# Performance work log

Hardware: AMD Instinct MI355X
Metric: run time of the kernel (lower is better)

The kernel has to match this reference:

```python
import jax, jax.numpy as jnp
import numpy as np

ATTEN_SIZE = 5  # half-window; module-global atten_size in source (0 there is non-functional)
B, S, D_IN, HID, OUT = 8, 2048, 512, 512, 2


def _xavier(key, shape):
    fan_in, fan_out = shape
    std = (2.0 / (fan_in + fan_out)) ** 0.5
    return jax.random.normal(key, shape, dtype=jnp.float32) * std


def setup_inputs() -> dict:
    key = jax.random.key(0)
    ks = jax.random.split(key, 8)
    return {
        "x": jax.random.normal(ks[0], (B, S, D_IN), dtype=jnp.float32),
        "W1": _xavier(ks[1], (D_IN, HID)),
        "b1": jnp.zeros((1, 1, HID), dtype=jnp.float32),
        "Wq": _xavier(ks[2], (HID, HID)),
        "Wk": _xavier(ks[3], (HID, HID)),
        "Wv": _xavier(ks[4], (HID, HID)),
        "W2": _xavier(ks[5], (HID, HID)),
        "b2": jnp.zeros((1, 1, HID), dtype=jnp.float32),
        "Wfc": _xavier(ks[6], (HID, OUT)),
        "bfc": jnp.zeros((OUT,), dtype=jnp.float32),
    }


def reference(x, W1, b1, Wq, Wk, Wv, W2, b2, Wfc, bfc):
    A = ATTEN_SIZE
    Wn = 2 * A + 1
    h = jax.nn.relu(x @ W1 + b1)                      # [B,S,H]
    b, s, hd = h.shape
    padded = jnp.pad(h, ((0, 0), (A, A), (0, 0)))     # [B,S+2A,H]
    # torch pad+roll(k)+stack+slice equals reversed window: x_nei[p, j] = padded[p + 2A - j]
    idx = jnp.arange(s)[:, None] + (2 * A - jnp.arange(Wn))[None, :]  # [S,Wn]
    x_nei = padded[:, idx, :]                         # [B,S,Wn,H]
    q = h @ Wq                                        # [B,S,H]
    k = x_nei @ Wk                                    # [B,S,Wn,H]
    v = x_nei @ Wv                                    # [B,S,Wn,H]
    scale = jnp.asarray(np.sqrt(float(hd)), dtype=h.dtype)
    scores = jnp.einsum('bsh,bswh->bsw', q, k)[:, :, None, :] / scale  # [B,S,1,Wn]
    # Faithful to torch.nn.Softmax(dim=2) on a singleton dim -> all ones
    w = jax.nn.softmax(scores, axis=2)                # [B,S,1,Wn]
    aw = jnp.einsum('bsjw,bswh->bsjh', w, v).reshape(b, s, hd)  # [B,S,H]
    out = jax.nn.relu(aw @ W2 + b2) @ Wfc + bfc       # [B,S,OUT]
    return out, aw
```

## Files before the change

### kernel.cpp

```cpp
#include <hip/hip_runtime.h>
#include <stdint.h>

#define B_   8
#define S_   2048
#define HID_ 512
#define M_   (B_ * S_)
#define AW_  5

typedef __attribute__((ext_vector_type(8))) short bf16x8;
typedef __attribute__((ext_vector_type(4))) float f32x4;
typedef unsigned short u16;

__device__ __forceinline__ u16 f2bf(float f) {
    uint32_t u = __builtin_bit_cast(uint32_t, f);
    u += 0x7FFFu + ((u >> 16) & 1u);
    return (u16)(u >> 16);
}
__device__ __forceinline__ float bf2f(u16 h) {
    uint32_t u = ((uint32_t)h) << 16;
    return __builtin_bit_cast(float, u);
}

__device__ __forceinline__ void gload16(const void* g, void* l) {
    __builtin_amdgcn_global_load_lds(
        (const __attribute__((address_space(1))) void*)(uintptr_t)g,
        (__attribute__((address_space(3))) void*)(uint32_t)(uintptr_t)l,
        16, 0, 0);
}

#define WAITV(n)  asm volatile("s_waitcnt vmcnt(" #n ")" ::: "memory")
#define WAITLG0() asm volatile("s_waitcnt lgkmcnt(0)" ::: "memory")

__global__ __launch_bounds__(256) void prep_w(const float* __restrict__ W1,
                                              const float* __restrict__ Wv,
                                              const float* __restrict__ W2,
                                              u16* __restrict__ W1t,
                                              u16* __restrict__ Wvt,
                                              u16* __restrict__ W2t,
                                              int do_w2) {
    const int wsel = blockIdx.x >> 8;
    if (wsel == 2 && !do_w2) return;
    const float* src = wsel == 0 ? W1 : (wsel == 1 ? Wv : W2);
    u16* dst = wsel == 0 ? W1t : (wsel == 1 ? Wvt : W2t);
    const int t  = blockIdx.x & 255;
    const int n0 = (t & 15) * 32, k0 = (t >> 4) * 32;
    __shared__ float tile[32][33];
    const int tr = threadIdx.x >> 5, tc = threadIdx.x & 31;
#pragma unroll
    for (int p = 0; p < 4; ++p)
        tile[tr + p * 8][tc] = src[(long)(k0 + tr + p * 8) * HID_ + n0 + tc];
    __syncthreads();
#pragma unroll
    for (int p = 0; p < 4; ++p)
        dst[(long)(n0 + tr + p * 8) * HID_ + k0 + tc] = f2bf(tile[tc][tr + p * 8]);
}

__global__ __launch_bounds__(256) void trans_w2(const float* __restrict__ W2,
                                                u16* __restrict__ W2t) {
    __shared__ float tile[32][33];
    const int k0 = blockIdx.y * 32, n0 = blockIdx.x * 32;
    const int tr = threadIdx.x >> 5, tc = threadIdx.x & 31;
#pragma unroll
    for (int p = 0; p < 4; ++p)
        tile[tr + p * 8][tc] = W2[(long)(k0 + tr + p * 8) * HID_ + n0 + tc];
    __syncthreads();
#pragma unroll
    for (int p = 0; p < 4; ++p)
        W2t[(long)(n0 + tr + p * 8) * HID_ + k0 + tc] = f2bf(tile[tc][tr + p * 8]);
}

__global__ __launch_bounds__(256, 2) void gemm1_f32a(const float* __restrict__ A,
                                                     const u16* __restrict__ Bt,
                                                     const float* __restrict__ bias,
                                                     u16* __restrict__ C) {
    __shared__ __attribute__((aligned(16))) u16 As[2][128 * 64];
    __shared__ __attribute__((aligned(16))) u16 Bs[2][128 * 64];

    const int tid = threadIdx.x;
    const int bid = blockIdx.x;
    const int swz = (bid & 7) * 64 + (bid >> 3);
    const int  bn   = (swz & 3) * 128;
    const long brow = (long)(swz >> 2) * 128;

    const int w  = tid >> 6;
    const int l  = tid & 63;
    const int wm = (w >> 1) * 64;
    const int wn = (w & 1) * 64;
    const int lr  = l & 15;
    const int lkb = (l >> 4) * 16;
    const int sw  = (lr & 7) << 4;

    const int r0 = tid >> 2;
    const int c0 = (tid & 3) * 16;
    const int r1 = 64 + r0;
    const float* ga0 = A + (brow + r0) * 512 + c0;
    const float* ga1 = A + (brow + r1) * 512 + c0;
    char* lw = (char*)&As[0][0];
    const int wb00 = r0 * 128 + ((c0 * 2 +  0) ^ ((r0 & 7) << 4));
    const int wb01 = r0 * 128 + ((c0 * 2 + 16) ^ ((r0 & 7) << 4));
    const int wb10 = r1 * 128 + ((c0 * 2 +  0) ^ ((r1 & 7) << 4));
    const int wb11 = r1 * 128 + ((c0 * 2 + 16) ^ ((r1 & 7) << 4));

    int pq[4];
    const u16* srcB[4];
#pragma unroll
    for (int q = 0; q < 4; ++q) {
        const int p   = tid * 16 + q * 4096;
        const int row = p >> 7;
        const int cb  = (p & 127) ^ ((row & 7) << 4);
        pq[q]   = p;
        srcB[q] = Bt + (long)(bn + row) * 512 + (cb >> 1);
    }

    f32x4 acc[4][4];
#pragma unroll
    for (int i = 0; i < 4; ++i)
#pragma unroll
        for (int j = 0; j < 4; ++j) {
            f32x4 z = {0.f, 0.f, 0.f, 0.f};
            acc[i][j] = z;
        }

    float4 ra[4], rb[4];

#define LOADA(k0)                                                        \
    {                                                                    \
        _Pragma("unroll") for (int u = 0; u < 4; ++u) {                  \
            ra[u] = *(const float4*)(ga0 + (k0) + u * 4);                \
            rb[u] = *(const float4*)(ga1 + (k0) + u * 4);                \
        }                                                                \
    }
#define CVTWRITE(buf)                                                    \
    {                                                                    \
        union { u16 u[8]; int4 v; } q0, q1, q2, q3;                      \
        q0.u[0]=f2bf(ra[0].x); q0.u[1]=f2bf(ra[0].y); q0.u[2]=f2bf(ra[0].z); q0.u[3]=f2bf(ra[0].w); \
        q0.u[4]=f2bf(ra[1].x); q0.u[5]=f2bf(ra[1].y); q0.u[6]=f2bf(ra[1].z); q0.u[7]=f2bf(ra[1].w); \
        q1.u[0]=f2bf(ra[2].x); q1.u[1]=f2bf(ra[2].y); q1.u[2]=f2bf(ra[2].z); q1.u[3]=f2bf(ra[2].w); \
        q1.u[4]=f2bf(ra[3].x); q1.u[5]=f2bf(ra[3].y); q1.u[6]=f2bf(ra[3].z); q1.u[7]=f2bf(ra[3].w); \
        q2.u[0]=f2bf(rb[0].x); q2.u[1]=f2bf(rb[0].y); q2.u[2]=f2bf(rb[0].z); q2.u[3]=f2bf(rb[0].w); \
        q2.u[4]=f2bf(rb[1].x); q2.u[5]=f2bf(rb[1].y); q2.u[6]=f2bf(rb[1].z); q2.u[7]=f2bf(rb[1].w); \
        q3.u[0]=f2bf(rb[2].x); q3.u[1]=f2bf(rb[2].y); q3.u[2]=f2bf(rb[2].z); q3.u[3]=f2bf(rb[2].w); \
        q3.u[4]=f2bf(rb[3].x); q3.u[5]=f2bf(rb[3].y); q3.u[6]=f2bf(rb[3].z); q3.u[7]=f2bf(rb[3].w); \
        *(int4*)(lw + (buf) * 16384 + wb00) = q0.v;                      \
        *(int4*)(lw + (buf) * 16384 + wb01) = q1.v;                      \
        *(int4*)(lw + (buf) * 16384 + wb10) = q2.v;                      \
        *(int4*)(lw + (buf) * 16384 + wb11) = q3.v;                      \
    }
#define STAGEB(buf, k0)                                                  \
    {                                                                    \
        _Pragma("unroll") for (int q = 0; q < 4; ++q)                    \
            gload16(srcB[q] + (k0), (char*)&Bs[buf][0] + pq[q]);         \
    }

    LOADA(0);
    STAGEB(0, 0);
    CVTWRITE(0);
    __syncthreads();

    int cur = 0;
    for (int t = 0; t < 8; ++t) {
        if (t < 7) {
            LOADA((t + 1) * 64);
            STAGEB(cur ^ 1, (t + 1) * 64);
        }
#pragma unroll
        for (int kk = 0; kk < 2; ++kk) {
            bf16x8 af[4], bfr[4];
#pragma unroll
            for (int i = 0; i < 4; ++i) {
                const int off = (wm + i * 16 + lr) * 128 + ((kk * 64 + lkb) ^ sw);
                af[i] = *(const bf16x8*)((const char*)&As[cur][0] + off);
            }
#pragma unroll
            for (int j = 0; j < 4; ++j) {
                const int off = (wn + j * 16 + lr) * 128 + ((kk * 64 + lkb) ^ sw);
                bfr[j] = *(const bf16x8*)((const char*)&Bs[cur][0] + off);
            }
#pragma unroll
            for (int i = 0; i < 4; ++i)
#pragma unroll
                for (int j = 0; j < 4; ++j)
                    acc[i][j] = __builtin_amdgcn_mfma_f32_16x16x32_bf16(
                        af[i], bfr[j], acc[i][j], 0, 0, 0);
        }
        if (t < 7) CVTWRITE(cur ^ 1);
        __syncthreads();
        cur ^= 1;
    }
#undef LOADA
#undef CVTWRITE
#undef STAGEB

    float bv[4];
#pragma unroll
    for (int j = 0; j < 4; ++j) bv[j] = bias[bn + wn + j * 16 + lr];
    const int rq = (l >> 4) * 4;
#pragma unroll
    for (int i = 0; i < 4; ++i)
#pragma unroll
        for (int q = 0; q < 4; ++q) {
            const long row = brow + wm + i * 16 + rq + q;
            u16* crow = C + row * 512 + bn + wn + lr;
#pragma unroll
            for (int j = 0; j < 4; ++j)
                crow[j * 16] = f2bf(fmaxf(acc[i][j][q] + bv[j], 0.f));
        }
}

template <int EPI>
__global__ __launch_bounds__(512, 2) void gemm256(const u16* __restrict__ A,
                                                  const u16* __restrict__ Bt,
                                                  const float* __restrict__ b2,
                                                  const float* __restrict__ Wfc,
                                                  u16* __restrict__ C,
                                                  float* __restrict__ partials) {
    __shared__ __attribute__((aligned(16))) u16 As[3][256 * 64];
    __shared__ __attribute__((aligned(16))) u16 Bs[3][128 * 64];

    const int tid = threadIdx.x;
    const int bid = blockIdx.x;
    const int swz = (bid & 7) * 32 + (bid >> 3);
    const int  bn   = (swz & 3) * 128;
    const long brow = (long)(swz >> 2) * 256;

    const int w  = tid >> 6;
    const int l  = tid & 63;
    const int wm = (w >> 2) * 128;
    const int wn = (w & 3) * 32;
    const int lr  = l & 15;
    const int lkb = (l >> 4) * 16;
    const int sw  = (lr & 7) << 4;

    int pa[4], pb[2];
    const u16* srcA[4];
    const u16* srcB[2];
#pragma unroll
    for (int q = 0; q < 4; ++q) {
        const int p   = tid * 16 + q * 8192;
        const int row = p >> 7;
        const int cb  = (p & 127) ^ ((row & 7) << 4);
        pa[q]   = p;
        srcA[q] = A + (brow + row) * 512 + (cb >> 1);
    }
#pragma unroll
    for (int q = 0; q < 2; ++q) {
        const int p   = tid * 16 + q * 8192;
        const int row = p >> 7;
        const int cb  = (p & 127) ^ ((row & 7) << 4);
        pb[q]   = p;
        srcB[q] = Bt + (long)(bn + row) * 512 + (cb >> 1);
    }

    f32x4 acc[8][2];
#pragma unroll
    for (int i = 0; i < 8; ++i)
#pragma unroll
        for (int j = 0; j < 2; ++j) {
            f32x4 z = {0.f, 0.f, 0.f, 0.f};
            acc[i][j] = z;
        }

#define STG(buf, k0)                                                     \
    {                                                                    \
        gload16(srcA[0] + (k0), (char*)&As[buf][0] + pa[0]);             \
        gload16(srcA[1] + (k0), (char*)&As[buf][0] + pa[1]);             \
        gload16(srcA[2] + (k0), (char*)&As[buf][0] + pa[2]);             \
        gload16(srcA[3] + (k0), (char*)&As[buf][0] + pa[3]);             \
        gload16(srcB[0] + (k0), (char*)&Bs[buf][0] + pb[0]);             \
        gload16(srcB[1] + (k0), (char*)&Bs[buf][0] + pb[1]);             \
    }

    STG(0, 0);
    STG(1, 64);
    WAITV(6);
    __builtin_amdgcn_s_barrier();

#pragma unroll
    for (int t = 0; t < 8; ++t) {
        if (t < 6) {
            const int nb = (t + 2) % 3;
            if (nb == 0)      STG(0, (t + 2) * 64)
            else if (nb == 1) STG(1, (t + 2) * 64)
            else              STG(2, (t + 2) * 64)
        }

        const int cbuf = t % 3;
        const char* ab = cbuf == 0 ? (const char*)&As[0][0]
                       : cbuf == 1 ? (const char*)&As[1][0] : (const char*)&As[2][0];
        const char* bb = cbuf == 0 ? (const char*)&Bs[0][0]
                       : cbuf == 1 ? (const char*)&Bs[1][0] : (const char*)&Bs[2][0];

        __builtin_amdgcn_s_setprio(1);
#pragma unroll
        for (int kk = 0; kk < 2; ++kk) {
            bf16x8 af[8], bfr[2];
#pragma unroll
            for (int j = 0; j < 2; ++j) {
                const int off = (wn + j * 16 + lr) * 128 + ((kk * 64 + lkb) ^ sw);
                bfr[j] = *(const bf16x8*)(bb + off);
            }
#pragma unroll
            for (int i = 0; i < 8; ++i) {
                const int off = (wm + i * 16 + lr) * 128 + ((kk * 64 + lkb) ^ sw);
                af[i] = *(const bf16x8*)(ab + off);
            }
#pragma unroll
            for (int i = 0; i < 8; ++i)
#pragma unroll
                for (int j = 0; j < 2; ++j)
                    acc[i][j] = __builtin_amdgcn_mfma_f32_16x16x32_bf16(
                        af[i], bfr[j], acc[i][j], 0, 0, 0);
        }
        __builtin_amdgcn_s_setprio(0);

        if (t < 7) {
            WAITLG0();
            __builtin_amdgcn_sched_barrier(0);
            if (t < 6) WAITV(6);
            else       WAITV(0);
            __builtin_amdgcn_s_barrier();
        }
    }
#undef STG

    const int rq = (l >> 4) * 4;
    if (EPI == 0) {
#pragma unroll
        for (int i = 0; i < 8; ++i)
#pragma unroll
            for (int q = 0; q < 4; ++q) {
                const long row = brow + wm + i * 16 + rq + q;
                u16* crow = C + row * 512 + bn + wn + lr;
#pragma unroll
                for (int j = 0; j < 2; ++j)
                    crow[j * 16] = f2bf(acc[i][j][q]);
            }
    } else {
        float bvv[2], w0v[2], w1v[2];
#pragma unroll
        for (int j = 0; j < 2; ++j) {
            const int col = bn + wn + j * 16 + lr;
            bvv[j] = b2[col];
            w0v[j] = Wfc[2 * col];
            w1v[j] = Wfc[2 * col + 1];
        }
        const int slot = (bn >> 7) * 4 + (w & 3);
#pragma unroll
        for (int i = 0; i < 8; ++i)
#pragma unroll
            for (int q = 0; q < 4; ++q) {
                float s0 = 0.f, s1 = 0.f;
#pragma unroll
                for (int j = 0; j < 2; ++j) {
                    const float v = fmaxf(acc[i][j][q] + bvv[j], 0.f);
                    s0 += v * w0v[j];
                    s1 += v * w1v[j];
                }
#pragma unroll
                for (int m = 1; m < 16; m <<= 1) {
                    s0 += __shfl_xor(s0, m);
                    s1 += __shfl_xor(s1, m);
                }
                if (lr == 0) {
                    const long row = brow + wm + i * 16 + rq + q;
                    float* pp = partials + ((long)slot * M_ + row) * 2;
                    pp[0] = s0;
                    pp[1] = s1;
                }
            }
    }
}

__global__ __launch_bounds__(256) void winsum_f(const u16* __restrict__ g,
                                                u16* __restrict__ awb,
                                                float* __restrict__ awf) {
    const long idx = (long)blockIdx.x * 256 + threadIdx.x;
    const int  c8  = (int)(idx & 63);
    const long bs  = idx >> 6;
    const int  s   = (int)(bs & (S_ - 1));

    float acc[8] = {};
#pragma unroll
    for (int d = -AW_; d <= AW_; ++d) {
        const int ss = s + d;
        if (0 <= ss && ss < S_) {
            const int4 v = *(const int4*)&g[(bs + d) * HID_ + c8 * 8];
            const u16* u = (const u16*)&v;
#pragma unroll
            for (int e = 0; e < 8; ++e) acc[e] += bf2f(u[e]);
        }
    }
    union { u16 u[8]; int4 v; } r;
#pragma unroll
    for (int e = 0; e < 8; ++e) r.u[e] = f2bf(acc[e]);
    *(int4*)&awb[bs * HID_ + c8 * 8] = r.v;
    float4 o0 = {acc[0], acc[1], acc[2], acc[3]};
    float4 o1 = {acc[4], acc[5], acc[6], acc[7]};
    *(float4*)&awf[bs * HID_ + c8 * 8]     = o0;
    *(float4*)&awf[bs * HID_ + c8 * 8 + 4] = o1;
}

__global__ __launch_bounds__(256) void fc_reduce(const float* __restrict__ partials,
                                                 const float* __restrict__ bfc,
                                                 float* __restrict__ out) {
    const int row = blockIdx.x * 256 + threadIdx.x;
    float s0 = bfc[0], s1 = bfc[1];
#pragma unroll
    for (int p = 0; p < 16; ++p) {
        s0 += partials[((long)p * M_ + row) * 2 + 0];
        s1 += partials[((long)p * M_ + row) * 2 + 1];
    }
    out[row * 2 + 0] = s0;
    out[row * 2 + 1] = s1;
}

extern "C" void kernel_launch(void* const* d_in, const int* in_sizes, int n_in,
                              void* d_out, int out_size, void* d_ws, size_t ws_size,
                              hipStream_t stream) {
    const float* x   = (const float*)d_in[0];
    const float* W1  = (const float*)d_in[1];
    const float* b1  = (const float*)d_in[2];
    const float* Wv  = (const float*)d_in[5];
    const float* W2  = (const float*)d_in[6];
    const float* b2  = (const float*)d_in[7];
    const float* Wfc = (const float*)d_in[8];
    const float* bfc = (const float*)d_in[9];

    float* out_part = (float*)d_out;
    float* aw_f32   = (float*)d_out + (long)M_ * 2;

    unsigned char* ws = (unsigned char*)d_ws;

    u16* W1t = (u16*)aw_f32;
    u16* Wvt = W1t + 262144;

    u16* h   = (u16*)ws;
    u16* g   = (u16*)ws + 8388608;
    u16* awb = h;
    float* partials = (float*)(ws + (17l << 20));

    const bool big = ws_size >= ((size_t)34 << 20);
    u16* W2t = big ? (u16*)(ws + (33l << 20)) : g;

    prep_w<<<768, 256, 0, stream>>>(W1, Wv, W2, W1t, Wvt, W2t, big ? 1 : 0);
    gemm1_f32a<<<512, 256, 0, stream>>>(x, W1t, b1, h);
    gemm256<0><<<256, 512, 0, stream>>>(h, Wvt, nullptr, nullptr, g, nullptr);
    winsum_f<<<4096, 256, 0, stream>>>(g, awb, aw_f32);
    if (!big)
        trans_w2<<<dim3(16, 16), 256, 0, stream>>>(W2, W2t);
    gemm256<1><<<256, 512, 0, stream>>>(awb, W2t, b2, Wfc, nullptr, partials);
    fc_reduce<<<64, 256, 0, stream>>>(partials, bfc, out_part);
}
```

Before: 79.76 us.

## Fuse window-sum into V-projection GEMM with halo rows; use 128-tile GEMM for W2

```diff
diff --git a/kernel.cpp b/kernel.cpp
--- a/kernel.cpp
+++ b/kernel.cpp
@@ -208,150 +208,119 @@
 }
 
 template <int EPI>
-__global__ __launch_bounds__(512, 2) void gemm256(const u16* __restrict__ A,
+__global__ __launch_bounds__(256, 2) void gemm128(const u16* __restrict__ A,
                                                   const u16* __restrict__ Bt,
                                                   const float* __restrict__ b2,
                                                   const float* __restrict__ Wfc,
                                                   u16* __restrict__ C,
                                                   float* __restrict__ partials) {
-    __shared__ __attribute__((aligned(16))) u16 As[3][256 * 64];
-    __shared__ __attribute__((aligned(16))) u16 Bs[3][128 * 64];
+    __shared__ __attribute__((aligned(16))) u16 As[2][128 * 64];
+    __shared__ __attribute__((aligned(16))) u16 Bs[2][128 * 64];
 
     const int tid = threadIdx.x;
     const int bid = blockIdx.x;
-    const int swz = (bid & 7) * 32 + (bid >> 3);
+    const int swz = (bid & 7) * 64 + (bid >> 3);
     const int  bn   = (swz & 3) * 128;
-    const long brow = (long)(swz >> 2) * 256;
+    const long brow = (long)(swz >> 2) * 128;
 
     const int w  = tid >> 6;
     const int l  = tid & 63;
-    const int wm = (w >> 2) * 128;
-    const int wn = (w & 3) * 32;
+    const int wm = (w >> 1) * 64;
+    const int wn = (w & 1) * 64;
     const int lr  = l & 15;
     const int lkb = (l >> 4) * 16;
     const int sw  = (lr & 7) << 4;
 
-    int pa[4], pb[2];
+    int pq[4];
     const u16* srcA[4];
-    const u16* srcB[2];
+    const u16* srcB[4];
 #pragma unroll
     for (int q = 0; q < 4; ++q) {
-        const int p   = tid * 16 + q * 8192;
+        const int p   = tid * 16 + q * 4096;
         const int row = p >> 7;
         const int cb  = (p & 127) ^ ((row & 7) << 4);
-        pa[q]   = p;
-        srcA[q] = A + (brow + row) * 512 + (cb >> 1);
-    }
-#pragma unroll
-    for (int q = 0; q < 2; ++q) {
-        const int p   = tid * 16 + q * 8192;
-        const int row = p >> 7;
-        const int cb  = (p & 127) ^ ((row & 7) << 4);
-        pb[q]   = p;
+        pq[q]   = p;
+        srcA[q] = A  + (brow + row) * 512 + (cb >> 1);
         srcB[q] = Bt + (long)(bn + row) * 512 + (cb >> 1);
     }
 
-    f32x4 acc[8][2];
-#pragma unroll
-    for (int i = 0; i < 8; ++i)
-#pragma unroll
-        for (int j = 0; j < 2; ++j) {
+    f32x4 acc[4][4];
+#pragma unroll
+    for (int i = 0; i < 4; ++i)
+#pragma unroll
+        for (int j = 0; j < 4; ++j) {
             f32x4 z = {0.f, 0.f, 0.f, 0.f};
             acc[i][j] = z;
         }
 
-#define STG(buf, k0)                                                     \
+#define STAGE(buf, k0)                                                   \
     {                                                                    \
-        gload16(srcA[0] + (k0), (char*)&As[buf][0] + pa[0]);             \
-        gload16(srcA[1] + (k0), (char*)&As[buf][0] + pa[1]);             \
-        gload16(srcA[2] + (k0), (char*)&As[buf][0] + pa[2]);             \
-        gload16(srcA[3] + (k0), (char*)&As[buf][0] + pa[3]);             \
-        gload16(srcB[0] + (k0), (char*)&Bs[buf][0] + pb[0]);             \
-        gload16(srcB[1] + (k0), (char*)&Bs[buf][0] + pb[1]);             \
-    }
-
-    STG(0, 0);
-    STG(1, 64);
-    WAITV(6);
-    __builtin_amdgcn_s_barrier();
-
-#pragma unroll
+        _Pragma("unroll") for (int q = 0; q < 4; ++q) {                  \
+            gload16(srcA[q] + (k0), (char*)&As[buf][0] + pq[q]);         \
+            gload16(srcB[q] + (k0), (char*)&Bs[buf][0] + pq[q]);         \
+        }                                                                \
+    }
+
+    int cur = 0;
+    STAGE(0, 0);
+    __syncthreads();
+
     for (int t = 0; t < 8; ++t) {
-        if (t < 6) {
-            const int nb = (t + 2) % 3;
-            if (nb == 0)      STG(0, (t + 2) * 64)
-            else if (nb == 1) STG(1, (t + 2) * 64)
-            else              STG(2, (t + 2) * 64)
-        }
-
-        const int cbuf = t % 3;
-        const char* ab = cbuf == 0 ? (const char*)&As[0][0]
-                       : cbuf == 1 ? (const char*)&As[1][0] : (const char*)&As[2][0];
-        const char* bb = cbuf == 0 ? (const char*)&Bs[0][0]
-                       : cbuf == 1 ? (const char*)&Bs[1][0] : (const char*)&Bs[2][0];
-
-        __builtin_amdgcn_s_setprio(1);
+        if (t < 7) STAGE(cur ^ 1, (t + 1) * 64);
 #pragma unroll
         for (int kk = 0; kk < 2; ++kk) {
-            bf16x8 af[8], bfr[2];
-#pragma unroll
-            for (int j = 0; j < 2; ++j) {
+            bf16x8 af[4], bfr[4];
+#pragma unroll
+            for (int i = 0; i < 4; ++i) {
+                const int off = (wm + i * 16 + lr) * 128 + ((kk * 64 + lkb) ^ sw);
+                af[i] = *(const bf16x8*)((const char*)&As[cur][0] + off);
+            }
+#pragma unroll
+            for (int j = 0; j < 4; ++j) {
                 const int off = (wn + j * 16 + lr) * 128 + ((kk * 64 + lkb) ^ sw);
-                bfr[j] = *(const bf16x8*)(bb + off);
-            }
-#pragma unroll
-            for (int i = 0; i < 8; ++i) {
-                const int off = (wm + i * 16 + lr) * 128 + ((kk * 64 + lkb) ^ sw);
-                af[i] = *(const bf16x8*)(ab + off);
-            }
-#pragma unroll
-            for (int i = 0; i < 8; ++i)
-#pragma unroll
-                for (int j = 0; j < 2; ++j)
+                bfr[j] = *(const bf16x8*)((const char*)&Bs[cur][0] + off);
+            }
+#pragma unroll
+            for (int i = 0; i < 4; ++i)
+#pragma unroll
+                for (int j = 0; j < 4; ++j)
                     acc[i][j] = __builtin_amdgcn_mfma_f32_16x16x32_bf16(
                         af[i], bfr[j], acc[i][j], 0, 0, 0);
         }
-        __builtin_amdgcn_s_setprio(0);
-
-        if (t < 7) {
-            WAITLG0();
-            __builtin_amdgcn_sched_barrier(0);
-            if (t < 6) WAITV(6);
-            else       WAITV(0);
-            __builtin_amdgcn_s_barrier();
-        }
-    }
-#undef STG
+        __syncthreads();
+        cur ^= 1;
+    }
+#undef STAGE
 
     const int rq = (l >> 4) * 4;
     if (EPI == 0) {
 #pragma unroll
-        for (int i = 0; i < 8; ++i)
+        for (int i = 0; i < 4; ++i)
 #pragma unroll
             for (int q = 0; q < 4; ++q) {
                 const long row = brow + wm + i * 16 + rq + q;
                 u16* crow = C + row * 512 + bn + wn + lr;
 #pragma unroll
-                for (int j = 0; j < 2; ++j)
+                for (int j = 0; j < 4; ++j)
                     crow[j * 16] = f2bf(acc[i][j][q]);
             }
     } else {
-        float bvv[2], w0v[2], w1v[2];
-#pragma unroll
-        for (int j = 0; j < 2; ++j) {
+        float bvv[4], w0v[4], w1v[4];
+#pragma unroll
+        for (int j = 0; j < 4; ++j) {
             const int col = bn + wn + j * 16 + lr;
             bvv[j] = b2[col];
             w0v[j] = Wfc[2 * col];
             w1v[j] = Wfc[2 * col + 1];
         }
-        const int slot = (bn >> 7) * 4 + (w & 3);
-#pragma unroll
-        for (int i = 0; i < 8; ++i)
+        const int slot = (bn >> 7) * 2 + (wn >> 6);
+#pragma unroll
+        for (int i = 0; i < 4; ++i)
 #pragma unroll
             for (int q = 0; q < 4; ++q) {
                 float s0 = 0.f, s1 = 0.f;
 #pragma unroll
-                for (int j = 0; j < 2; ++j) {
+                for (int j = 0; j < 4; ++j) {
                     const float v = fmaxf(acc[i][j][q] + bvv[j], 0.f);
                     s0 += v * w0v[j];
                     s1 += v * w1v[j];
@@ -371,6 +340,175 @@
     }
 }
 
+__global__ __launch_bounds__(512, 2) void gemm2_ws(const u16* __restrict__ A,
+                                                   const u16* __restrict__ Bt,
+                                                   u16* __restrict__ awb,
+                                                   float* __restrict__ awf) {
+    __shared__ __attribute__((aligned(16))) u16 As[3][288 * 64];
+    __shared__ __attribute__((aligned(16))) u16 Bs[3][128 * 64];
+
+    const int tid = threadIdx.x;
+    const int bid = blockIdx.x;
+    const int swz = (bid & 7) * 32 + (bid >> 3);
+    const int  bn   = (swz & 3) * 128;
+    const long brow = (long)(swz >> 2) * 256;
+
+    const int w  = tid >> 6;
+    const int l  = tid & 63;
+    const int wm = (w >> 2) * 144;
+    const int wn = (w & 3) * 32;
+    const int lr  = l & 15;
+    const int lkb = (l >> 4) * 16;
+    const int sw  = (lr & 7) << 4;
+    const bool loww = (tid < 256);
+
+    int pa[5];
+    const u16* srcA[5];
+#pragma unroll
+    for (int q = 0; q < 4; ++q) {
+        const int p   = tid * 16 + q * 8192;
+        const int row = p >> 7;
+        const int cb  = (p & 127) ^ ((row & 7) << 4);
+        long R = brow - 16 + row;
+        R = R < 0 ? 0 : (R > M_ - 1 ? M_ - 1 : R);
+        pa[q]   = p;
+        srcA[q] = A + R * 512 + (cb >> 1);
+    }
+    pa[4] = 0; srcA[4] = A;
+    if (loww) {
+        const int p   = 32768 + tid * 16;
+        const int row = p >> 7;
+        const int cb  = (p & 127) ^ ((row & 7) << 4);
+        long R = brow - 16 + row;
+        R = R < 0 ? 0 : (R > M_ - 1 ? M_ - 1 : R);
+        pa[4]   = p;
+        srcA[4] = A + R * 512 + (cb >> 1);
+    }
+    int pb[2];
+    const u16* srcB[2];
+#pragma unroll
+    for (int q = 0; q < 2; ++q) {
+        const int p   = tid * 16 + q * 8192;
+        const int row = p >> 7;
+        const int cb  = (p & 127) ^ ((row & 7) << 4);
+        pb[q]   = p;
+        srcB[q] = Bt + (long)(bn + row) * 512 + (cb >> 1);
+    }
+
+    f32x4 acc[9][2];
+#pragma unroll
+    for (int i = 0; i < 9; ++i)
+#pragma unroll
+        for (int j = 0; j < 2; ++j) {
+            f32x4 z = {0.f, 0.f, 0.f, 0.f};
+            acc[i][j] = z;
+        }
+
+#define STG(buf, k0)                                                     \
+    {                                                                    \
+        gload16(srcA[0] + (k0), (char*)&As[buf][0] + pa[0]);             \
+        gload16(srcA[1] + (k0), (char*)&As[buf][0] + pa[1]);             \
+        gload16(srcA[2] + (k0), (char*)&As[buf][0] + pa[2]);             \
+        gload16(srcA[3] + (k0), (char*)&As[buf][0] + pa[3]);             \
+        if (loww) gload16(srcA[4] + (k0), (char*)&As[buf][0] + pa[4]);   \
+        gload16(srcB[0] + (k0), (char*)&Bs[buf][0] + pb[0]);             \
+        gload16(srcB[1] + (k0), (char*)&Bs[buf][0] + pb[1]);             \
+    }
+#define WAITP()                                                          \
+    do {                                                                 \
+        if (loww) { WAITV(7); } else { WAITV(6); }                       \
+    } while (0)
+
+    STG(0, 0);
+    STG(1, 64);
+    WAITP();
+    __builtin_amdgcn_s_barrier();
+
+#pragma unroll
+    for (int t = 0; t < 8; ++t) {
+        if (t < 6) {
+            const int nb = (t + 2) % 3;
+            if (nb == 0)      STG(0, (t + 2) * 64)
+            else if (nb == 1) STG(1, (t + 2) * 64)
+            else              STG(2, (t + 2) * 64)
+        }
+
+        const int cbuf = t % 3;
+        const char* ab = cbuf == 0 ? (const char*)&As[0][0]
+                       : cbuf == 1 ? (const char*)&As[1][0] : (const char*)&As[2][0];
+        const char* bb = cbuf == 0 ? (const char*)&Bs[0][0]
+                       : cbuf == 1 ? (const char*)&Bs[1][0] : (const char*)&Bs[2][0];
+
+        __builtin_amdgcn_s_setprio(1);
+#pragma unroll
+        for (int kk = 0; kk < 2; ++kk) {
+            bf16x8 af[9], bfr[2];
+#pragma unroll
+            for (int j = 0; j < 2; ++j) {
+                const int off = (wn + j * 16 + lr) * 128 + ((kk * 64 + lkb) ^ sw);
+                bfr[j] = *(const bf16x8*)(bb + off);
+            }
+#pragma unroll
+            for (int i = 0; i < 9; ++i) {
+                const int off = (wm + i * 16 + lr) * 128 + ((kk * 64 + lkb) ^ sw);
+                af[i] = *(const bf16x8*)(ab + off);
+            }
+#pragma unroll
+            for (int i = 0; i < 9; ++i)
+#pragma unroll
+                for (int j = 0; j < 2; ++j)
+                    acc[i][j] = __builtin_amdgcn_mfma_f32_16x16x32_bf16(
+                        af[i], bfr[j], acc[i][j], 0, 0, 0);
+        }
+        __builtin_amdgcn_s_setprio(0);
+
+        if (t < 7) {
+            WAITLG0();
+            __builtin_amdgcn_sched_barrier(0);
+            if (t < 6) { WAITP(); } else { WAITV(0); }
+            __builtin_amdgcn_s_barrier();
+        }
+    }
+#undef STG
+#undef WAITP
+
+    __syncthreads();
+    u16* gl = &As[0][0];
+
+    const int rq4 = (l >> 4) * 4;
+#pragma unroll
+    for (int i = 0; i < 9; ++i)
+#pragma unroll
+        for (int j = 0; j < 2; ++j)
+#pragma unroll
+            for (int q = 0; q < 4; ++q) {
+                const int row = wm + i * 16 + rq4 + q;
+                const int col = wn + j * 16 + lr;
+                gl[row * 128 + col] = f2bf(acc[i][j][q]);
+            }
+    __syncthreads();
+
+    for (int rr = 0; rr < 32; ++rr) {
+        const int  rloc = w * 32 + rr;
+        const long R    = brow + rloc;
+        const int  s    = (int)(R & (S_ - 1));
+        float a0 = 0.f, a1 = 0.f;
+#pragma unroll
+        for (int d = -AW_; d <= AW_; ++d) {
+            if ((unsigned)(s + d) < (unsigned)S_) {
+                const uint32_t v =
+                    *(const uint32_t*)&gl[(rloc + 16 + d) * 128 + 2 * l];
+                a0 += bf2f((u16)(v & 0xffffu));
+                a1 += bf2f((u16)(v >> 16));
+            }
+        }
+        const uint32_t pk = (uint32_t)f2bf(a0) | ((uint32_t)f2bf(a1) << 16);
+        *(uint32_t*)&awb[R * 512 + bn + 2 * l] = pk;
+        float2 o; o.x = a0; o.y = a1;
+        *(float2*)&awf[R * 512 + bn + 2 * l] = o;
+    }
+}
+
 __global__ __launch_bounds__(256) void winsum_f(const u16* __restrict__ g,
                                                 u16* __restrict__ awb,
                                                 float* __restrict__ awf) {
@@ -406,7 +544,7 @@
     const int row = blockIdx.x * 256 + threadIdx.x;
     float s0 = bfc[0], s1 = bfc[1];
 #pragma unroll
-    for (int p = 0; p < 16; ++p) {
+    for (int p = 0; p < 8; ++p) {
         s0 += partials[((long)p * M_ + row) * 2 + 0];
         s1 += partials[((long)p * M_ + row) * 2 + 1];
     }
@@ -431,23 +569,36 @@
 
     unsigned char* ws = (unsigned char*)d_ws;
 
-    u16* W1t = (u16*)aw_f32;
-    u16* Wvt = W1t + 262144;
-
-    u16* h   = (u16*)ws;
-    u16* g   = (u16*)ws + 8388608;
-    u16* awb = h;
-    float* partials = (float*)(ws + (17l << 20));
-
-    const bool big = ws_size >= ((size_t)34 << 20);
-    u16* W2t = big ? (u16*)(ws + (33l << 20)) : g;
-
-    prep_w<<<768, 256, 0, stream>>>(W1, Wv, W2, W1t, Wvt, W2t, big ? 1 : 0);
-    gemm1_f32a<<<512, 256, 0, stream>>>(x, W1t, b1, h);
-    gemm256<0><<<256, 512, 0, stream>>>(h, Wvt, nullptr, nullptr, g, nullptr);
-    winsum_f<<<4096, 256, 0, stream>>>(g, awb, aw_f32);
-    if (!big)
+    const bool big = ws_size >= ((size_t)35 << 20);
+
+    if (big) {
+        u16* h    = (u16*)ws;
+        u16* awb  = (u16*)(ws + (16l << 20));
+        u16* W1t  = (u16*)(ws + (32l << 20));
+        u16* Wvt  = W1t + 262144;
+        u16* W2t  = Wvt + 262144;
+        float* partials = (float*)(ws + (33l << 20) + (1l << 19));
+
+        prep_w<<<768, 256, 0, stream>>>(W1, Wv, W2, W1t, Wvt, W2t, 1);
+        gemm1_f32a<<<512, 256, 0, stream>>>(x, W1t, b1, h);
+        gemm2_ws<<<256, 512, 0, stream>>>(h, Wvt, awb, aw_f32);
+        gemm128<1><<<512, 256, 0, stream>>>(awb, W2t, b2, Wfc, nullptr, partials);
+        fc_reduce<<<64, 256, 0, stream>>>(partials, bfc, out_part);
+    } else {
+        u16* W1t = (u16*)aw_f32;
+        u16* Wvt = W1t + 262144;
+        u16* h   = (u16*)ws;
+        u16* g   = (u16*)ws + 8388608;
+        u16* awb = h;
+        u16* W2t = g;
+        float* partials = (float*)(ws + (17l << 20));
+
+        prep_w<<<768, 256, 0, stream>>>(W1, Wv, W2, W1t, Wvt, W2t, 0);
+        gemm1_f32a<<<512, 256, 0, stream>>>(x, W1t, b1, h);
+        gemm128<0><<<512, 256, 0, stream>>>(h, Wvt, nullptr, nullptr, g, nullptr);
+        winsum_f<<<4096, 256, 0, stream>>>(g, awb, aw_f32);
         trans_w2<<<dim3(16, 16), 256, 0, stream>>>(W2, W2t);
-    gemm256<1><<<256, 512, 0, stream>>>(awb, W2t, b2, Wfc, nullptr, partials);
-    fc_reduce<<<64, 256, 0, stream>>>(partials, bfc, out_part);
-}
+        gemm128<1><<<512, 256, 0, stream>>>(awb, W2t, b2, Wfc, nullptr, partials);
+        fc_reduce<<<64, 256, 0, stream>>>(partials, bfc, out_part);
+    }
+}
```

Result: faster. 75.43 us, median of 2 (-5.4%).
